# Kernel tuning notes

Hardware: AMD Instinct MI355X
Metric: run time of the kernel (lower is better)

The kernel has to match this reference:

```python
import jax, jax.numpy as jnp
import numpy as np

N_EMBD = 1024
N_HEAD = 16
HEAD_DIM = N_EMBD // N_HEAD

def setup_inputs() -> dict:
    key = jax.random.key(0)
    ks = jax.random.split(key, 5)
    B, T, C = 2, 2048, N_EMBD
    s = 1.0 / np.sqrt(C)
    x = jax.random.normal(ks[0], (B, T, C), dtype=jnp.float32)
    W_qkv = jax.random.normal(ks[1], (C, 3 * C), dtype=jnp.float32) * s
    b_qkv = jax.random.normal(ks[2], (3 * C,), dtype=jnp.float32) * 0.02
    W_o = jax.random.normal(ks[3], (C, C), dtype=jnp.float32) * s
    b_o = jax.random.normal(ks[4], (C,), dtype=jnp.float32) * 0.02
    return {"x": x, "W_qkv": W_qkv, "b_qkv": b_qkv, "W_o": W_o, "b_o": b_o}

def reference(x, W_qkv, b_qkv, W_o, b_o):
    B, T, C = x.shape
    H, D = N_HEAD, HEAD_DIM
    scale = 1.0 / np.sqrt(D)
    qkv = jnp.einsum('btc,cf->btf', x, W_qkv) + b_qkv  # [B,T,3C]
    q, k, v = jnp.split(qkv, 3, axis=-1)
    # [B,H,T,D]
    q = q.reshape(B, T, H, D).transpose(0, 2, 1, 3)
    k = k.reshape(B, T, H, D).transpose(0, 2, 1, 3)
    v = v.reshape(B, T, H, D).transpose(0, 2, 1, 3)
    att = jnp.einsum('bhqd,bhkd->bhqk', q, k) * scale  # [B,H,T,T]
    causal = jnp.tril(jnp.ones((T, T), dtype=bool))
    att = jnp.where(causal[None, None], att, -jnp.inf)
    att = jax.nn.softmax(att, axis=-1)
    y = jnp.einsum('bhqk,bhkd->bhqd', att, v)  # [B,H,T,D]
    y = y.transpose(0, 2, 1, 3).reshape(B, T, C)
    return jnp.einsum('btc,cf->btf', y, W_o) + b_o
```

## Files before the change

### kernel.cpp

```cpp
#include <hip/hip_runtime.h>
#include <hip/hip_bf16.h>

#define TT 2048
#define BB 2
#define CC 1024
#define NH 16
#define HD 64

typedef __attribute__((ext_vector_type(8))) short short8;
typedef __attribute__((ext_vector_type(4))) short short4b;
typedef __attribute__((ext_vector_type(4))) float f32x4;

typedef unsigned int __attribute__((address_space(1))) ui_gas;
typedef unsigned int __attribute__((address_space(3))) ui_las;

#if __has_builtin(__builtin_amdgcn_mfma_f32_16x16x16bf16_1k)
#define PV16 1
#define VSS 4
#else
#define PV16 0
#define VSS 8
#endif

__device__ __forceinline__ float us2f(unsigned short u) {
    union { unsigned int i; float f; } v; v.i = ((unsigned int)u) << 16; return v.f;
}
__device__ __forceinline__ unsigned short f2us(float f) {
    union { float f; unsigned int i; } v; v.f = f;
    unsigned int i = v.i;
    unsigned int lsb = (i >> 16) & 1u;
    i += 0x7fffu + lsb;
    return (unsigned short)(i >> 16);
}
__device__ __forceinline__ unsigned int pack2_trunc(float a, float b) {
    union { float f; unsigned int u; } x, y; x.f = a; y.f = b;
    return (y.u & 0xffff0000u) | (x.u >> 16);
}

__device__ __forceinline__ void gl_lds16(const unsigned short* g, unsigned short* l) {
    __builtin_amdgcn_global_load_lds((const ui_gas*)g, (ui_las*)l, 16, 0, 0);
}

__device__ __forceinline__ float4 load4(const void* p, size_t i, int isbf) {
    if (isbf) {
        ushort4 u = *reinterpret_cast<const ushort4*>((const unsigned short*)p + i);
        return make_float4(us2f(u.x), us2f(u.y), us2f(u.z), us2f(u.w));
    } else {
        return *reinterpret_cast<const float4*>((const float*)p + i);
    }
}
__device__ __forceinline__ float load1(const void* p, size_t i, int isbf) {
    return isbf ? us2f(((const unsigned short*)p)[i]) : ((const float*)p)[i];
}

__global__ __launch_bounds__(256) void prep_kernel(
    const void* __restrict__ x, const void* __restrict__ Wqkv, const void* __restrict__ Wo,
    const void* __restrict__ bqkv, const void* __restrict__ bo,
    unsigned short* __restrict__ xb, unsigned short* __restrict__ Wqkvt,
    unsigned short* __restrict__ Wot, int* __restrict__ flags)
{
    __shared__ float Ls[64 * 65];
    __shared__ int sh_isbf;
    const int t = threadIdx.x;
    const int bid = blockIdx.x;

    const void* src;
    int mode, sub;
    if (bid < 2048)      { mode = 0; sub = bid;        src = x; }
    else if (bid < 2816) { mode = 1; sub = bid - 2048; src = Wqkv; }
    else                 { mode = 2; sub = bid - 2816; src = Wo; }

    if (bid == 0 && t < 64) {
        const void* ps[5] = {x, Wqkv, bqkv, Wo, bo};
        for (int k = 0; k < 5; ++k) {
            const unsigned short* u = (const unsigned short*)ps[k];
            int bad = 0;
            #pragma unroll
            for (int j = 0; j < 4; ++j) {
                float v = us2f(u[t * 4 + j]);
                if (!(fabsf(v) < 1e4f)) bad = 1;
            }
            unsigned long long m = __ballot(bad != 0);
            if (t == 0) flags[k] = (__popcll(m) < 4) ? 1 : 0;
        }
    }
    if (t < 64) {
        const unsigned short* u = (const unsigned short*)src;
        int bad = 0;
        #pragma unroll
        for (int j = 0; j < 4; ++j) {
            float v = us2f(u[t * 4 + j]);
            if (!(fabsf(v) < 1e4f)) bad = 1;
        }
        unsigned long long m = __ballot(bad != 0);
        if (t == 0) sh_isbf = (__popcll(m) < 4) ? 1 : 0;
    }
    __syncthreads();
    const int isbf = sh_isbf;

    if (mode == 0) {
        const size_t i = ((size_t)sub * 256 + t) * 8;
        float4 a = load4(src, i, isbf);
        float4 b = load4(src, i + 4, isbf);
        alignas(16) unsigned short pk[8];
        pk[0] = f2us(a.x); pk[1] = f2us(a.y); pk[2] = f2us(a.z); pk[3] = f2us(a.w);
        pk[4] = f2us(b.x); pk[5] = f2us(b.y); pk[6] = f2us(b.z); pk[7] = f2us(b.w);
        *reinterpret_cast<uint4*>(xb + i) = *reinterpret_cast<const uint4*>(pk);
        return;
    }

    int N, Krows, n0, k0;
    unsigned short* dst;
    if (mode == 1) { N = 3 * CC; Krows = CC; dst = Wqkvt; n0 = (sub % 48) * 64; k0 = (sub / 48) * 64; }
    else           { N = CC;     Krows = CC; dst = Wot;   n0 = (sub % 16) * 64; k0 = (sub / 16) * 64; }
    {
        const int r = t >> 2, cq = (t & 3) << 4;
        #pragma unroll
        for (int i = 0; i < 4; ++i) {
            float4 v = load4(src, (size_t)(k0 + r) * N + n0 + cq + i * 4, isbf);
            Ls[r * 65 + cq + i * 4 + 0] = v.x;
            Ls[r * 65 + cq + i * 4 + 1] = v.y;
            Ls[r * 65 + cq + i * 4 + 2] = v.z;
            Ls[r * 65 + cq + i * 4 + 3] = v.w;
        }
    }
    __syncthreads();
    {
        const int c = t & 63, kg = (t >> 6) * 16;
        alignas(16) unsigned short pk[16];
        #pragma unroll
        for (int i = 0; i < 16; ++i) pk[i] = f2us(Ls[(kg + i) * 65 + c]);
        unsigned short* d = dst + (size_t)(n0 + c) * Krows + k0 + kg;
        *reinterpret_cast<uint4*>(d + 0) = *reinterpret_cast<const uint4*>(&pk[0]);
        *reinterpret_cast<uint4*>(d + 8) = *reinterpret_cast<const uint4*>(&pk[8]);
    }
}

template<int WM, int WN, int NWM, int NWN>
__global__ __launch_bounds__(256) void gemm_mfma(
    const unsigned short* __restrict__ A,
    const unsigned short* __restrict__ Bt,
    const void* __restrict__ bias, void* __restrict__ C,
    int M, int N, int K,
    const int* __restrict__ flags, int biasfi, int cfi)
{
    constexpr int BM = WM * 16 * NWM, BN = WN * 16 * NWN;
    constexpr int ASL = BM / 16, BSL = BN / 16;

    const int bias_bf = (biasfi >= 0) ? flags[biasfi] : 0;
    const int c_bf    = (cfi >= 0) ? flags[cfi] : ((cfi == -2) ? 1 : 0);

    __shared__ __align__(16) unsigned short Asl[ASL * 2 * 512];
    __shared__ __align__(16) unsigned short Bsl[BSL * 2 * 512];

    const int tid = threadIdx.x;
    const int l  = tid & 63;
    const int w  = tid >> 6;
    const int wm = w / NWN, wn = w % NWN;
    const int bm = blockIdx.y * BM, bn = blockIdx.x * BN;
    const int lm = l & 15;
    const int lk = (l >> 4) * 8;

    f32x4 acc[WM][WN];
    #pragma unroll
    for (int i = 0; i < WM; ++i)
        #pragma unroll
        for (int j = 0; j < WN; ++j) acc[i][j] = (f32x4){0.f, 0.f, 0.f, 0.f};

    for (int k0 = 0; k0 < K; k0 += 64) {
        #pragma unroll
        for (int s = 0; s < ASL / 4; ++s) {
            const int r = w * (ASL / 4) + s;
            #pragma unroll
            for (int kh = 0; kh < 2; ++kh)
                gl_lds16(A + (size_t)(bm + r * 16 + lm) * K + k0 + kh * 32 + lk,
                         &Asl[(r * 2 + kh) * 512]);
        }
        #pragma unroll
        for (int s = 0; s < BSL / 4; ++s) {
            const int r = w * (BSL / 4) + s;
            #pragma unroll
            for (int kh = 0; kh < 2; ++kh)
                gl_lds16(Bt + (size_t)(bn + r * 16 + lm) * K + k0 + kh * 32 + lk,
                         &Bsl[(r * 2 + kh) * 512]);
        }
        __syncthreads();
        #pragma unroll
        for (int kh = 0; kh < 2; ++kh) {
            short8 af[WM], bf[WN];
            #pragma unroll
            for (int i = 0; i < WM; ++i)
                af[i] = *reinterpret_cast<const short8*>(&Asl[((WM * wm + i) * 2 + kh) * 512 + l * 8]);
            #pragma unroll
            for (int j = 0; j < WN; ++j)
                bf[j] = *reinterpret_cast<const short8*>(&Bsl[((WN * wn + j) * 2 + kh) * 512 + l * 8]);
            #pragma unroll
            for (int i = 0; i < WM; ++i)
                #pragma unroll
                for (int j = 0; j < WN; ++j)
                    acc[i][j] = __builtin_amdgcn_mfma_f32_16x16x32_bf16(af[i], bf[j], acc[i][j], 0, 0, 0);
        }
        __syncthreads();
    }

    const int quad = l >> 4;
    float bv[WN];
    #pragma unroll
    for (int j = 0; j < WN; ++j) bv[j] = load1(bias, bn + (WN * wn + j) * 16 + lm, bias_bf);

    #pragma unroll
    for (int i = 0; i < WM; ++i) {
        #pragma unroll
        for (int r = 0; r < 4; ++r) {
            const int row = bm + (WM * wm + i) * 16 + quad * 4 + r;
            #pragma unroll
            for (int j = 0; j < WN; ++j) {
                const int col = bn + (WN * wn + j) * 16 + lm;
                const float val = acc[i][j][r] + bv[j];
                if (c_bf) ((unsigned short*)C)[(size_t)row * N + col] = f2us(val);
                else      ((float*)C)[(size_t)row * N + col] = val;
            }
        }
    }
}

__global__ __launch_bounds__(256) void transpose_v(
    const unsigned short* __restrict__ qkv, unsigned short* __restrict__ Vt)
{
    __shared__ __align__(16) unsigned short Ls[64 * 72];
    const int tid = threadIdx.x;
    const int tt = blockIdx.x;
    const int bh = blockIdx.y;
    const int b = bh >> 4, h = bh & 15;
    {
        const int tok = tid & 63, w = tid >> 6;
        const unsigned short* src = qkv + (size_t)(b * TT + tt * 64 + tok) * 3 * CC + 2 * CC + h * HD;
        #pragma unroll
        for (int c2 = 0; c2 < 2; ++c2) {
            int c = 2 * w + c2;
            uint4 d = *(const uint4*)(src + c * 8);
            *(uint4*)(&Ls[tok * 72 + c * 8]) = d;
        }
    }
    __syncthreads();
    {
        const int d = tid >> 2, kq = tid & 3;
        unsigned short out[16];
        #pragma unroll
        for (int i = 0; i < 16; ++i) out[i] = Ls[(kq * 16 + i) * 72 + d];
        unsigned short* dst = Vt + (size_t)bh * HD * TT + (size_t)d * TT + tt * 64 + kq * 16;
        *(uint4*)(dst + 0) = *(uint4*)(&out[0]);
        *(uint4*)(dst + 8) = *(uint4*)(&out[8]);
    }
}

__global__ __launch_bounds__(256) void attn_mfma(
    const unsigned short* __restrict__ qkv,
    const unsigned short* __restrict__ Vt,
    unsigned short* __restrict__ y)
{
    __shared__ __align__(16) unsigned short Ksh[8 * 512];
    __shared__ __align__(16) unsigned short Vsh[1039 * VSS];

    const int tid = threadIdx.x;
    const int l   = tid & 63;
    const int w   = tid >> 6;
    const int quad = l >> 4;
    const int col  = l & 15;

    const int n  = blockIdx.x;
    const int g  = n >> 3;
    const int bh = (n & 7) * 4 + (g & 3);
    const int i  = g >> 2;
    const int tA = i, tB = 31 - i;
    const int b  = bh >> 4, h = bh & 15;

#if !PV16
    for (int ss = tid; ss < 1039; ss += 256)
        *(uint2*)(&Vsh[ss * 8 + 4]) = make_uint2(0u, 0u);
#endif

    const float QSCALE = 0.18033688f;
    short8 qfA[2], qfB[2];
    #pragma unroll
    for (int t2 = 0; t2 < 2; ++t2) {
        const int qt = t2 ? tB : tA;
        short8* qf = t2 ? qfB : qfA;
        const int token = qt * 64 + w * 16 + col;
        const unsigned short* qrow = qkv + (size_t)(b * TT + token) * 3 * CC + h * HD;
        #pragma unroll
        for (int ks = 0; ks < 2; ++ks) {
            ushort4 u0 = *(const ushort4*)(qrow + ks * 32 + quad * 8);
            ushort4 u1 = *(const ushort4*)(qrow + ks * 32 + quad * 8 + 4);
            alignas(16) unsigned short pk[8];
            pk[0] = f2us(us2f(u0.x) * QSCALE);
            pk[1] = f2us(us2f(u0.y) * QSCALE);
            pk[2] = f2us(us2f(u0.z) * QSCALE);
            pk[3] = f2us(us2f(u0.w) * QSCALE);
            pk[4] = f2us(us2f(u1.x) * QSCALE);
            pk[5] = f2us(us2f(u1.y) * QSCALE);
            pk[6] = f2us(us2f(u1.z) * QSCALE);
            pk[7] = f2us(us2f(u1.w) * QSCALE);
            qf[ks] = *(const short8*)pk;
        }
    }

    f32x4 oA[4], oB[4];
    #pragma unroll
    for (int nb = 0; nb < 4; ++nb) {
        oA[nb] = (f32x4){0.f, 0.f, 0.f, 0.f};
        oB[nb] = (f32x4){0.f, 0.f, 0.f, 0.f};
    }
    float lAc = 0.f, lBc = 0.f;

    const unsigned short* kbase = qkv + (size_t)b * TT * 3 * CC + CC + h * HD;
    const unsigned short* vbase = Vt + (size_t)bh * HD * TT;

    const int vd = tid >> 2, vg0 = (tid & 3) * 4;

    uint4 rk[2], rv[2];
    auto issue_loads = [&](int kt) {
        const unsigned short* ksrc = kbase + (size_t)(kt * 64 + l) * 3 * CC;
        #pragma unroll
        for (int c2 = 0; c2 < 2; ++c2) {
            const int c = 2 * w + c2;
            rk[c2] = *(const uint4*)(ksrc + c * 8);
        }
        const unsigned short* vsrc = vbase + (size_t)vd * TT + kt * 64 + vg0 * 4;
        rv[0] = *(const uint4*)(vsrc + 0);
        rv[1] = *(const uint4*)(vsrc + 8);
    };
    auto write_lds = [&]() {
        #pragma unroll
        for (int c2 = 0; c2 < 2; ++c2) {
            const int c = 2 * w + c2;
            const int ks = c >> 2, q = c & 3;
            const int slot = ((quad * 2 + ks) * 64 + q * 16 + col) * 8;
            *(uint4*)(&Ksh[slot]) = rk[c2];
        }
        *(uint2*)(&Vsh[((vg0 + 0) * 65 + vd) * VSS]) = make_uint2(rv[0].x, rv[0].y);
        *(uint2*)(&Vsh[((vg0 + 1) * 65 + vd) * VSS]) = make_uint2(rv[0].z, rv[0].w);
        *(uint2*)(&Vsh[((vg0 + 2) * 65 + vd) * VSS]) = make_uint2(rv[1].x, rv[1].y);
        *(uint2*)(&Vsh[((vg0 + 3) * 65 + vd) * VSS]) = make_uint2(rv[1].z, rv[1].w);
    };

    auto step = [&](const short8* qf, f32x4* o, float& l_i, bool diag) {
        f32x4 st[4];
        #pragma unroll
        for (int nb = 0; nb < 4; ++nb) {
            f32x4 acc = {0.f, 0.f, 0.f, 0.f};
            #pragma unroll
            for (int ks = 0; ks < 2; ++ks) {
                short8 kf = *(const short8*)(&Ksh[((nb * 2 + ks) * 64 + l) * 8]);
                acc = __builtin_amdgcn_mfma_f32_16x16x32_bf16(kf, qf[ks], acc, 0, 0, 0);
            }
            st[nb] = acc;
        }
        float pv[4][4];
        float rs = 0.f;
        #pragma unroll
        for (int nb = 0; nb < 4; ++nb)
            #pragma unroll
            for (int r = 0; r < 4; ++r) {
                float v = st[nb][r];
                if (diag && (nb * 16 + quad * 4 + r > w * 16 + col)) v = -3e38f;
                float p = __builtin_exp2f(v);
                pv[nb][r] = p;
                rs += p;
            }
        rs += __shfl_xor(rs, 16);
        rs += __shfl_xor(rs, 32);
        l_i += rs;
#if PV16
        short4b pf[4];
        #pragma unroll
        for (int nbk = 0; nbk < 4; ++nbk) {
            union { short4b s; unsigned int u[2]; } pk;
            pk.u[0] = pack2_trunc(pv[nbk][0], pv[nbk][1]);
            pk.u[1] = pack2_trunc(pv[nbk][2], pv[nbk][3]);
            pf[nbk] = pk.s;
        }
        #pragma unroll
        for (int nbd = 0; nbd < 4; ++nbd)
            #pragma unroll
            for (int nbk = 0; nbk < 4; ++nbk) {
                short4b vf = *(const short4b*)(&Vsh[((nbk * 4 + quad) * 65 + nbd * 16 + col) * VSS]);
                o[nbd] = __builtin_amdgcn_mfma_f32_16x16x16bf16_1k(pf[nbk], vf, o[nbd], 0, 0, 0);
            }
#else
        short8 pf[4];
        #pragma unroll
        for (int nbk = 0; nbk < 4; ++nbk) {
            union { short8 s; unsigned int u[4]; } pk;
            pk.u[0] = pack2_trunc(pv[nbk][0], pv[nbk][1]);
            pk.u[1] = pack2_trunc(pv[nbk][2], pv[nbk][3]);
            pk.u[2] = 0u; pk.u[3] = 0u;
            pf[nbk] = pk.s;
        }
        #pragma unroll
        for (int nbd = 0; nbd < 4; ++nbd)
            #pragma unroll
            for (int nbk = 0; nbk < 4; ++nbk) {
                short8 vf = *(const short8*)(&Vsh[((nbk * 4 + quad) * 65 + nbd * 16 + col) * VSS]);
                o[nbd] = __builtin_amdgcn_mfma_f32_16x16x32_bf16(pf[nbk], vf, o[nbd], 0, 0, 0);
            }
#endif
    };

    issue_loads(0);
    for (int kt = 0; kt <= tB; ++kt) {
        write_lds();
        __syncthreads();
        if (kt < tB) issue_loads(kt + 1);
        step(qfB, oB, lBc, kt == tB);
        if (kt <= tA) step(qfA, oA, lAc, kt == tA);
        __syncthreads();
    }

    #pragma unroll
    for (int t2 = 0; t2 < 2; ++t2) {
        const int qt = t2 ? tB : tA;
        f32x4* o = t2 ? oB : oA;
        const float inv = 1.f / (t2 ? lBc : lAc);
        float invr[4];
        #pragma unroll
        for (int r = 0; r < 4; ++r) invr[r] = __shfl(inv, quad * 4 + r);
        #pragma unroll
        for (int nb = 0; nb < 4; ++nb)
            #pragma unroll
            for (int r = 0; r < 4; ++r) {
                int token = qt * 64 + w * 16 + quad * 4 + r;
                y[(size_t)(b * TT + token) * CC + h * HD + nb * 16 + col] = f2us(o[nb][r] * invr[r]);
            }
    }
}

extern "C" void kernel_launch(void* const* d_in, const int* in_sizes, int n_in,
                              void* d_out, int out_size, void* d_ws, size_t ws_size,
                              hipStream_t stream) {
    const int M = BB * TT;

    char* ws = (char*)d_ws;
    int*            flags = (int*)ws;                         ws += 256;
    unsigned short* xb    = (unsigned short*)ws;              ws += (size_t)M * CC * 2;
    unsigned short* Wqkvt = (unsigned short*)ws;              ws += (size_t)3 * CC * CC * 2;
    unsigned short* Wot   = (unsigned short*)ws;              ws += (size_t)CC * CC * 2;
    unsigned short* qkv   = (unsigned short*)ws;              ws += (size_t)M * 3 * CC * 2;
    unsigned short* Vt    = (unsigned short*)ws;              ws += (size_t)BB * NH * HD * TT * 2;
    unsigned short* y     = (unsigned short*)ws;

    prep_kernel<<<3072, 256, 0, stream>>>(d_in[0], d_in[1], d_in[3], d_in[2], d_in[4],
                                          xb, Wqkvt, Wot, flags);

    gemm_mfma<4, 4, 2, 2><<<dim3(3 * CC / 128, M / 128), 256, 0, stream>>>(
        xb, Wqkvt, d_in[2], qkv, M, 3 * CC, CC, flags, 2, -2);

    transpose_v<<<dim3(TT / 64, BB * NH), 256, 0, stream>>>(qkv, Vt);

    attn_mfma<<<512, 256, 0, stream>>>(qkv, Vt, y);

    gemm_mfma<2, 4, 4, 1><<<dim3(CC / 64, M / 128), 256, 0, stream>>>(
        y, Wot, d_in[4], d_out, M, CC, CC, flags, 4, 0);
}
```

Before: 230.7 us.

## Split paired-tile attention blocks into single-tile blocks with double-buffered LDS

The attention kernel now gives each block a single query tile instead of a balanced pair (tA, 31-tA), doubling the grid to 1024 blocks. A longest-first block ordering keeps the load balanced. The K/V LDS tiles are double-buffered, so one barrier per iteration suffices and the next tile's global loads overlap compute. A launch-bounds occupancy hint of 4 is added. The cost is that each K/V tile is loaded from global memory twice as often overall (no reuse across two query tiles), and the LDS footprint doubles.

```diff
diff --git a/kernel.cpp b/kernel.cpp
--- a/kernel.cpp
+++ b/kernel.cpp
@@ -254,13 +254,13 @@
     }
 }
 
-__global__ __launch_bounds__(256) void attn_mfma(
+__global__ __launch_bounds__(256, 4) void attn_mfma(
     const unsigned short* __restrict__ qkv,
     const unsigned short* __restrict__ Vt,
     unsigned short* __restrict__ y)
 {
-    __shared__ __align__(16) unsigned short Ksh[8 * 512];
-    __shared__ __align__(16) unsigned short Vsh[1039 * VSS];
+    __shared__ __align__(16) unsigned short Ksh[2][8 * 512];
+    __shared__ __align__(16) unsigned short Vsh[2][1039 * VSS];
 
     const int tid = threadIdx.x;
     const int l   = tid & 63;
@@ -269,24 +269,28 @@
     const int col  = l & 15;
 
     const int n  = blockIdx.x;
-    const int g  = n >> 3;
-    const int bh = (n & 7) * 4 + (g & 3);
-    const int i  = g >> 2;
-    const int tA = i, tB = 31 - i;
+    const int bh = n & 31;
+    const int j0 = (n >> 5) & 7;
+    const int kk = (n >> 8) & 3;
+    int i;
+    if      (kk == 0) i = 31 - j0;
+    else if (kk == 1) i = j0;
+    else if (kk == 2) i = 16 + j0;
+    else              i = 15 - j0;
     const int b  = bh >> 4, h = bh & 15;
 
 #if !PV16
-    for (int ss = tid; ss < 1039; ss += 256)
-        *(uint2*)(&Vsh[ss * 8 + 4]) = make_uint2(0u, 0u);
+    {
+        unsigned short* vflat = &Vsh[0][0];
+        for (int ss = tid; ss < 1039 * 2; ss += 256)
+            *(uint2*)(&vflat[ss * 8 + 4]) = make_uint2(0u, 0u);
+    }
 #endif
 
     const float QSCALE = 0.18033688f;
-    short8 qfA[2], qfB[2];
-    #pragma unroll
-    for (int t2 = 0; t2 < 2; ++t2) {
-        const int qt = t2 ? tB : tA;
-        short8* qf = t2 ? qfB : qfA;
-        const int token = qt * 64 + w * 16 + col;
+    short8 qf[2];
+    {
+        const int token = i * 64 + w * 16 + col;
         const unsigned short* qrow = qkv + (size_t)(b * TT + token) * 3 * CC + h * HD;
         #pragma unroll
         for (int ks = 0; ks < 2; ++ks) {
@@ -305,13 +309,10 @@
         }
     }
 
-    f32x4 oA[4], oB[4];
+    f32x4 o[4];
     #pragma unroll
-    for (int nb = 0; nb < 4; ++nb) {
-        oA[nb] = (f32x4){0.f, 0.f, 0.f, 0.f};
-        oB[nb] = (f32x4){0.f, 0.f, 0.f, 0.f};
-    }
-    float lAc = 0.f, lBc = 0.f;
+    for (int nb = 0; nb < 4; ++nb) o[nb] = (f32x4){0.f, 0.f, 0.f, 0.f};
+    float lc = 0.f;
 
     const unsigned short* kbase = qkv + (size_t)b * TT * 3 * CC + CC + h * HD;
     const unsigned short* vbase = Vt + (size_t)bh * HD * TT;
@@ -330,28 +331,28 @@
         rv[0] = *(const uint4*)(vsrc + 0);
         rv[1] = *(const uint4*)(vsrc + 8);
     };
-    auto write_lds = [&]() {
+    auto write_lds = [&](int bb) {
         #pragma unroll
         for (int c2 = 0; c2 < 2; ++c2) {
             const int c = 2 * w + c2;
             const int ks = c >> 2, q = c & 3;
             const int slot = ((quad * 2 + ks) * 64 + q * 16 + col) * 8;
-            *(uint4*)(&Ksh[slot]) = rk[c2];
-        }
-        *(uint2*)(&Vsh[((vg0 + 0) * 65 + vd) * VSS]) = make_uint2(rv[0].x, rv[0].y);
-        *(uint2*)(&Vsh[((vg0 + 1) * 65 + vd) * VSS]) = make_uint2(rv[0].z, rv[0].w);
-        *(uint2*)(&Vsh[((vg0 + 2) * 65 + vd) * VSS]) = make_uint2(rv[1].x, rv[1].y);
-        *(uint2*)(&Vsh[((vg0 + 3) * 65 + vd) * VSS]) = make_uint2(rv[1].z, rv[1].w);
+            *(uint4*)(&Ksh[bb][slot]) = rk[c2];
+        }
+        *(uint2*)(&Vsh[bb][((vg0 + 0) * 65 + vd) * VSS]) = make_uint2(rv[0].x, rv[0].y);
+        *(uint2*)(&Vsh[bb][((vg0 + 1) * 65 + vd) * VSS]) = make_uint2(rv[0].z, rv[0].w);
+        *(uint2*)(&Vsh[bb][((vg0 + 2) * 65 + vd) * VSS]) = make_uint2(rv[1].x, rv[1].y);
+        *(uint2*)(&Vsh[bb][((vg0 + 3) * 65 + vd) * VSS]) = make_uint2(rv[1].z, rv[1].w);
     };
 
-    auto step = [&](const short8* qf, f32x4* o, float& l_i, bool diag) {
+    auto step = [&](bool diag, int bb) {
         f32x4 st[4];
         #pragma unroll
         for (int nb = 0; nb < 4; ++nb) {
             f32x4 acc = {0.f, 0.f, 0.f, 0.f};
             #pragma unroll
             for (int ks = 0; ks < 2; ++ks) {
-                short8 kf = *(const short8*)(&Ksh[((nb * 2 + ks) * 64 + l) * 8]);
+                short8 kf = *(const short8*)(&Ksh[bb][((nb * 2 + ks) * 64 + l) * 8]);
                 acc = __builtin_amdgcn_mfma_f32_16x16x32_bf16(kf, qf[ks], acc, 0, 0, 0);
             }
             st[nb] = acc;
@@ -370,7 +371,7 @@
             }
         rs += __shfl_xor(rs, 16);
         rs += __shfl_xor(rs, 32);
-        l_i += rs;
+        lc += rs;
 #if PV16
         short4b pf[4];
         #pragma unroll
@@ -384,7 +385,7 @@
         for (int nbd = 0; nbd < 4; ++nbd)
             #pragma unroll
             for (int nbk = 0; nbk < 4; ++nbk) {
-                short4b vf = *(const short4b*)(&Vsh[((nbk * 4 + quad) * 65 + nbd * 16 + col) * VSS]);
+                short4b vf = *(const short4b*)(&Vsh[bb][((nbk * 4 + quad) * 65 + nbd * 16 + col) * VSS]);
                 o[nbd] = __builtin_amdgcn_mfma_f32_16x16x16bf16_1k(pf[nbk], vf, o[nbd], 0, 0, 0);
             }
 #else
@@ -401,27 +402,25 @@
         for (int nbd = 0; nbd < 4; ++nbd)
             #pragma unroll
             for (int nbk = 0; nbk < 4; ++nbk) {
-                short8 vf = *(const short8*)(&Vsh[((nbk * 4 + quad) * 65 + nbd * 16 + col) * VSS]);
+                short8 vf = *(const short8*)(&Vsh[bb][((nbk * 4 + quad) * 65 + nbd * 16 + col) * VSS]);
                 o[nbd] = __builtin_amdgcn_mfma_f32_16x16x32_bf16(pf[nbk], vf, o[nbd], 0, 0, 0);
             }
 #endif
     };
 
     issue_loads(0);
-    for (int kt = 0; kt <= tB; ++kt) {
-        write_lds();
+    write_lds(0);
+    __syncthreads();
+    for (int kt = 0; kt <= i; ++kt) {
+        const int cur = kt & 1;
+        if (kt < i) issue_loads(kt + 1);
+        step(kt == i, cur);
+        if (kt < i) write_lds(cur ^ 1);
         __syncthreads();
-        if (kt < tB) issue_loads(kt + 1);
-        step(qfB, oB, lBc, kt == tB);
-        if (kt <= tA) step(qfA, oA, lAc, kt == tA);
-        __syncthreads();
-    }
-
-    #pragma unroll
-    for (int t2 = 0; t2 < 2; ++t2) {
-        const int qt = t2 ? tB : tA;
-        f32x4* o = t2 ? oB : oA;
-        const float inv = 1.f / (t2 ? lBc : lAc);
+    }
+
+    {
+        const float inv = 1.f / lc;
         float invr[4];
         #pragma unroll
         for (int r = 0; r < 4; ++r) invr[r] = __shfl(inv, quad * 4 + r);
@@ -429,7 +428,7 @@
         for (int nb = 0; nb < 4; ++nb)
             #pragma unroll
             for (int r = 0; r < 4; ++r) {
-                int token = qt * 64 + w * 16 + quad * 4 + r;
+                int token = i * 64 + w * 16 + quad * 4 + r;
                 y[(size_t)(b * TT + token) * CC + h * HD + nb * 16 + col] = f2us(o[nb][r] * invr[r]);
             }
     }
@@ -457,7 +456,7 @@
 
     transpose_v<<<dim3(TT / 64, BB * NH), 256, 0, stream>>>(qkv, Vt);
 
-    attn_mfma<<<512, 256, 0, stream>>>(qkv, Vt, y);
+    attn_mfma<<<1024, 256, 0, stream>>>(qkv, Vt, y);
 
     gemm_mfma<2, 4, 4, 1><<<dim3(CC / 64, M / 128), 256, 0, stream>>>(
         y, Wot, d_in[4], d_out, M, CC, CC, flags, 4, 0);
```

Result: slower. 253.4 us (+9.8%).

## Fuse V transpose into QKV GEMM epilogue and double-buffer attention LDS

Applied to the files above, without the earlier changes.

The QKV GEMM epilogue now also writes V columns directly into the transposed Vt layout, which removes the separate transpose_v kernel launch and its extra read of qkv. The attention kernel double-buffers its K/V shared-memory tiles, so the next tile is written to LDS after compute and one barrier per iteration is dropped. The risks are that the Vt scatter writes are strided 2-byte stores, which may be poorly coalesced, and that doubled LDS use can lower occupancy.

```diff
diff --git a/kernel.cpp b/kernel.cpp
--- a/kernel.cpp
+++ b/kernel.cpp
@@ -141,6 +141,7 @@
     const unsigned short* __restrict__ A,
     const unsigned short* __restrict__ Bt,
     const void* __restrict__ bias, void* __restrict__ C,
+    unsigned short* __restrict__ Vt,
     int M, int N, int K,
     const int* __restrict__ flags, int biasfi, int cfi)
 {
@@ -217,40 +218,20 @@
             for (int j = 0; j < WN; ++j) {
                 const int col = bn + (WN * wn + j) * 16 + lm;
                 const float val = acc[i][j][r] + bv[j];
-                if (c_bf) ((unsigned short*)C)[(size_t)row * N + col] = f2us(val);
-                else      ((float*)C)[(size_t)row * N + col] = val;
-            }
-        }
-    }
-}
-
-__global__ __launch_bounds__(256) void transpose_v(
-    const unsigned short* __restrict__ qkv, unsigned short* __restrict__ Vt)
-{
-    __shared__ __align__(16) unsigned short Ls[64 * 72];
-    const int tid = threadIdx.x;
-    const int tt = blockIdx.x;
-    const int bh = blockIdx.y;
-    const int b = bh >> 4, h = bh & 15;
-    {
-        const int tok = tid & 63, w = tid >> 6;
-        const unsigned short* src = qkv + (size_t)(b * TT + tt * 64 + tok) * 3 * CC + 2 * CC + h * HD;
-        #pragma unroll
-        for (int c2 = 0; c2 < 2; ++c2) {
-            int c = 2 * w + c2;
-            uint4 d = *(const uint4*)(src + c * 8);
-            *(uint4*)(&Ls[tok * 72 + c * 8]) = d;
-        }
-    }
-    __syncthreads();
-    {
-        const int d = tid >> 2, kq = tid & 3;
-        unsigned short out[16];
-        #pragma unroll
-        for (int i = 0; i < 16; ++i) out[i] = Ls[(kq * 16 + i) * 72 + d];
-        unsigned short* dst = Vt + (size_t)bh * HD * TT + (size_t)d * TT + tt * 64 + kq * 16;
-        *(uint4*)(dst + 0) = *(uint4*)(&out[0]);
-        *(uint4*)(dst + 8) = *(uint4*)(&out[8]);
+                if (c_bf) {
+                    const unsigned short us = f2us(val);
+                    ((unsigned short*)C)[(size_t)row * N + col] = us;
+                    if (Vt != nullptr && col >= 2 * CC) {
+                        const int cc2 = col - 2 * CC;
+                        const int h = cc2 >> 6, d = cc2 & 63;
+                        const int bq = row / TT, tk = row % TT;
+                        Vt[((size_t)(bq * NH + h) * HD + d) * TT + tk] = us;
+                    }
+                } else {
+                    ((float*)C)[(size_t)row * N + col] = val;
+                }
+            }
+        }
     }
 }
 
@@ -259,8 +240,8 @@
     const unsigned short* __restrict__ Vt,
     unsigned short* __restrict__ y)
 {
-    __shared__ __align__(16) unsigned short Ksh[8 * 512];
-    __shared__ __align__(16) unsigned short Vsh[1039 * VSS];
+    __shared__ __align__(16) unsigned short Ksh[2][8 * 512];
+    __shared__ __align__(16) unsigned short Vsh[2][1039 * VSS];
 
     const int tid = threadIdx.x;
     const int l   = tid & 63;
@@ -276,8 +257,11 @@
     const int b  = bh >> 4, h = bh & 15;
 
 #if !PV16
-    for (int ss = tid; ss < 1039; ss += 256)
-        *(uint2*)(&Vsh[ss * 8 + 4]) = make_uint2(0u, 0u);
+    {
+        unsigned short* vflat = &Vsh[0][0];
+        for (int ss = tid; ss < 1039 * 2; ss += 256)
+            *(uint2*)(&vflat[ss * 8 + 4]) = make_uint2(0u, 0u);
+    }
 #endif
 
     const float QSCALE = 0.18033688f;
@@ -330,28 +314,28 @@
         rv[0] = *(const uint4*)(vsrc + 0);
         rv[1] = *(const uint4*)(vsrc + 8);
     };
-    auto write_lds = [&]() {
+    auto write_lds = [&](int bb) {
         #pragma unroll
         for (int c2 = 0; c2 < 2; ++c2) {
             const int c = 2 * w + c2;
             const int ks = c >> 2, q = c & 3;
             const int slot = ((quad * 2 + ks) * 64 + q * 16 + col) * 8;
-            *(uint4*)(&Ksh[slot]) = rk[c2];
-        }
-        *(uint2*)(&Vsh[((vg0 + 0) * 65 + vd) * VSS]) = make_uint2(rv[0].x, rv[0].y);
-        *(uint2*)(&Vsh[((vg0 + 1) * 65 + vd) * VSS]) = make_uint2(rv[0].z, rv[0].w);
-        *(uint2*)(&Vsh[((vg0 + 2) * 65 + vd) * VSS]) = make_uint2(rv[1].x, rv[1].y);
-        *(uint2*)(&Vsh[((vg0 + 3) * 65 + vd) * VSS]) = make_uint2(rv[1].z, rv[1].w);
+            *(uint4*)(&Ksh[bb][slot]) = rk[c2];
+        }
+        *(uint2*)(&Vsh[bb][((vg0 + 0) * 65 + vd) * VSS]) = make_uint2(rv[0].x, rv[0].y);
+        *(uint2*)(&Vsh[bb][((vg0 + 1) * 65 + vd) * VSS]) = make_uint2(rv[0].z, rv[0].w);
+        *(uint2*)(&Vsh[bb][((vg0 + 2) * 65 + vd) * VSS]) = make_uint2(rv[1].x, rv[1].y);
+        *(uint2*)(&Vsh[bb][((vg0 + 3) * 65 + vd) * VSS]) = make_uint2(rv[1].z, rv[1].w);
     };
 
-    auto step = [&](const short8* qf, f32x4* o, float& l_i, bool diag) {
+    auto step = [&](const short8* qf, f32x4* o, float& l_i, bool diag, int bb) {
         f32x4 st[4];
         #pragma unroll
         for (int nb = 0; nb < 4; ++nb) {
             f32x4 acc = {0.f, 0.f, 0.f, 0.f};
             #pragma unroll
             for (int ks = 0; ks < 2; ++ks) {
-                short8 kf = *(const short8*)(&Ksh[((nb * 2 + ks) * 64 + l) * 8]);
+                short8 kf = *(const short8*)(&Ksh[bb][((nb * 2 + ks) * 64 + l) * 8]);
                 acc = __builtin_amdgcn_mfma_f32_16x16x32_bf16(kf, qf[ks], acc, 0, 0, 0);
             }
             st[nb] = acc;
@@ -384,7 +368,7 @@
         for (int nbd = 0; nbd < 4; ++nbd)
             #pragma unroll
             for (int nbk = 0; nbk < 4; ++nbk) {
-                short4b vf = *(const short4b*)(&Vsh[((nbk * 4 + quad) * 65 + nbd * 16 + col) * VSS]);
+                short4b vf = *(const short4b*)(&Vsh[bb][((nbk * 4 + quad) * 65 + nbd * 16 + col) * VSS]);
                 o[nbd] = __builtin_amdgcn_mfma_f32_16x16x16bf16_1k(pf[nbk], vf, o[nbd], 0, 0, 0);
             }
 #else
@@ -401,19 +385,21 @@
         for (int nbd = 0; nbd < 4; ++nbd)
             #pragma unroll
             for (int nbk = 0; nbk < 4; ++nbk) {
-                short8 vf = *(const short8*)(&Vsh[((nbk * 4 + quad) * 65 + nbd * 16 + col) * VSS]);
+                short8 vf = *(const short8*)(&Vsh[bb][((nbk * 4 + quad) * 65 + nbd * 16 + col) * VSS]);
                 o[nbd] = __builtin_amdgcn_mfma_f32_16x16x32_bf16(pf[nbk], vf, o[nbd], 0, 0, 0);
             }
 #endif
     };
 
     issue_loads(0);
+    write_lds(0);
+    __syncthreads();
     for (int kt = 0; kt <= tB; ++kt) {
-        write_lds();
-        __syncthreads();
+        const int cur = kt & 1;
         if (kt < tB) issue_loads(kt + 1);
-        step(qfB, oB, lBc, kt == tB);
-        if (kt <= tA) step(qfA, oA, lAc, kt == tA);
+        step(qfB, oB, lBc, kt == tB, cur);
+        if (kt <= tA) step(qfA, oA, lAc, kt == tA, cur);
+        if (kt < tB) write_lds(cur ^ 1);
         __syncthreads();
     }
 
@@ -453,12 +439,10 @@
                                           xb, Wqkvt, Wot, flags);
 
     gemm_mfma<4, 4, 2, 2><<<dim3(3 * CC / 128, M / 128), 256, 0, stream>>>(
-        xb, Wqkvt, d_in[2], qkv, M, 3 * CC, CC, flags, 2, -2);
-
-    transpose_v<<<dim3(TT / 64, BB * NH), 256, 0, stream>>>(qkv, Vt);
+        xb, Wqkvt, d_in[2], qkv, Vt, M, 3 * CC, CC, flags, 2, -2);
 
     attn_mfma<<<512, 256, 0, stream>>>(qkv, Vt, y);
 
     gemm_mfma<2, 4, 4, 1><<<dim3(CC / 64, M / 128), 256, 0, stream>>>(
-        y, Wot, d_in[4], d_out, M, CC, CC, flags, 4, 0);
-}
+        y, Wot, d_in[4], d_out, nullptr, M, CC, CC, flags, 4, 0);
+}
```

Result: no change. 230.2 us (-0.2%).
